# Performance work log

Measured on AMD Instinct MI355X. Metric: run time of the kernel, lower is better.

The kernel has to match this reference:

```python
import jax, jax.numpy as jnp
import numpy as np

B, N, D_IN, D_H, D_OUT, H = 16384, 32, 128, 128, 128, 4

def setup_inputs() -> dict:
    key = jax.random.key(0)
    ks = jax.random.split(key, 7)
    s_in = 1.0 / np.sqrt(D_IN)
    s_h = 1.0 / np.sqrt(D_H)
    return {
        "x": jax.random.normal(ks[0], (B, 1, D_IN), dtype=jnp.float32),
        "neighbors": jax.random.normal(ks[1], (B, N, D_IN), dtype=jnp.float32),
        "Wq": jax.random.uniform(ks[2], (H, D_H, D_IN), jnp.float32, -s_in, s_in),
        "Wk": jax.random.uniform(ks[3], (H, D_H, D_IN), jnp.float32, -s_in, s_in),
        "Wv": jax.random.uniform(ks[4], (H, D_H, D_IN), jnp.float32, -s_in, s_in),
        "Wo": jax.random.uniform(ks[5], (D_OUT, D_H), jnp.float32, -s_h, s_h),
        "bo": jax.random.uniform(ks[6], (D_OUT,), jnp.float32, -s_h, s_h),
    }

def reference(x, neighbors, Wq, Wk, Wv, Wo, bo):
    # Per-head projections (torch Linear: y = x @ W.T), batched over heads
    q = jnp.einsum("bqi,hdi->bhqd", x, Wq)          # [B,H,1,Dh]
    k = jnp.einsum("bni,hdi->bhnd", neighbors, Wk)  # [B,H,N,Dh]
    v = jnp.einsum("bni,hdi->bhnd", neighbors, Wv)  # [B,H,N,Dh]
    logits = jnp.einsum("bhqd,bhnd->bhqn", q, k)    # [B,H,1,N]
    attn = jax.nn.softmax(logits, axis=-1)
    # Sum over heads (original accumulates res += per head), then average
    res = jnp.einsum("bhqn,bhnd->bqd", attn, v) / q.shape[1]  # [B,1,Dh]
    out = jnp.einsum("bqd,od->bqo", res, Wo) + bo
    out = jax.nn.leaky_relu(out, negative_slope=0.01)
    return out[:, 0, :]  # squeeze(1) -> [B, D_OUT]
```

## Files before the change

kernel.cpp:

```cpp
#include <hip/hip_runtime.h>
#include <hip/hip_bf16.h>
#include <cstddef>

#define NBATCH 16384
#define NNB 32
#define DD 128
#define NH 4
#define NHD 512
#define NT 512
#define BPB 8

typedef __attribute__((ext_vector_type(8))) short short8v;
typedef __attribute__((ext_vector_type(4))) float f32x4;

__device__ __forceinline__ unsigned f2bf1(float f) {
  unsigned u = __float_as_uint(f);
  return (u + 0x7FFFu + ((u >> 16) & 1u)) >> 16;
}
__device__ __forceinline__ unsigned pack2bf(float lo, float hi) {
  return f2bf1(lo) | (f2bf1(hi) << 16);
}
__device__ __forceinline__ float bflo(unsigned u) { return __uint_as_float(u << 16); }
__device__ __forceinline__ float bfhi(unsigned u) { return __uint_as_float(u & 0xFFFF0000u); }

__global__ __launch_bounds__(256) void precompute_kernel(
    const float* __restrict__ Wq, const float* __restrict__ Wk,
    const float* __restrict__ Wv, const float* __restrict__ Wo,
    unsigned short* __restrict__ AAfh, unsigned short* __restrict__ AAfl,
    unsigned short* __restrict__ CCf) {
  int e = blockIdx.x * 256 + threadIdx.x;
  if (blockIdx.y == 0) {
    int i = e >> 9;
    int hd = e & 511;
    int h = hd >> 7, d = hd & 127;
    const float* wq = Wq + h * 16384;
    const float* wk = Wk + h * 16384;
    float acc = 0.f;
    #pragma unroll 8
    for (int r = 0; r < 128; ++r) acc += wq[r * 128 + i] * wk[r * 128 + d];
    int t2 = hd >> 4;
    int ks = i >> 5, kg = (i >> 3) & 3, eo = i & 7;
    int lane = (hd & 15) + 16 * kg;
    size_t idx = ((size_t)(t2 * 4 + ks) * 64 + lane) * 8 + eo;
    unsigned hv = f2bf1(acc);
    AAfh[idx] = (unsigned short)hv;
    AAfl[idx] = (unsigned short)f2bf1(acc - __uint_as_float(hv << 16));
  } else {
    int k = e >> 7;
    int o = e & 127;
    int h = k >> 7, i = k & 127;
    const float* wv = Wv + h * 16384;
    float acc = 0.f;
    #pragma unroll 8
    for (int d = 0; d < 128; ++d) acc += Wo[o * 128 + d] * wv[d * 128 + i];
    int t = o >> 4, s = k >> 5, g = (k >> 3) & 3, eo = k & 7;
    int lane = (o & 15) + 16 * g;
    size_t idx = ((size_t)(t * 16 + s) * 64 + lane) * 8 + eo;
    CCf[idx] = (unsigned short)f2bf1(0.25f * acc);
  }
}

__global__ __launch_bounds__(512) void gemm1_kernel(
    const float* __restrict__ x, const unsigned short* __restrict__ AAfh,
    const unsigned short* __restrict__ AAfl, unsigned* __restrict__ Gf32) {
  __shared__ __align__(16) float x_lds[32][132];
  const int t = threadIdx.x;
  const size_t B0 = (size_t)blockIdx.x * 32;
  {
    const float4* src = (const float4*)(x + B0 * DD);
    #pragma unroll
    for (int j = 0; j < 2; ++j) {
      int flat = j * 512 + t;
      float4 f = src[flat];
      int b = flat >> 5, c4 = flat & 31;
      *(float4*)&x_lds[b][c4 * 4] = f;
    }
  }
  __syncthreads();
  const int w = t >> 6, l = t & 63;
  const int hm = l & 15, kg = l >> 4;
  const int mt = w & 1;
  const int q = w >> 1;

  short8v xh[4], xl[4];
  #pragma unroll
  for (int ks = 0; ks < 4; ++ks) {
    float4 a = *(const float4*)&x_lds[mt * 16 + hm][ks * 32 + kg * 8];
    float4 b = *(const float4*)&x_lds[mt * 16 + hm][ks * 32 + kg * 8 + 4];
    unsigned h0 = f2bf1(a.x), h1 = f2bf1(a.y), h2 = f2bf1(a.z), h3 = f2bf1(a.w);
    unsigned h4 = f2bf1(b.x), h5 = f2bf1(b.y), h6 = f2bf1(b.z), h7 = f2bf1(b.w);
    union { unsigned u[4]; short8v v; } H, L;
    H.u[0] = h0 | (h1 << 16); H.u[1] = h2 | (h3 << 16);
    H.u[2] = h4 | (h5 << 16); H.u[3] = h6 | (h7 << 16);
    L.u[0] = pack2bf(a.x - __uint_as_float(h0 << 16), a.y - __uint_as_float(h1 << 16));
    L.u[1] = pack2bf(a.z - __uint_as_float(h2 << 16), a.w - __uint_as_float(h3 << 16));
    L.u[2] = pack2bf(b.x - __uint_as_float(h4 << 16), b.y - __uint_as_float(h5 << 16));
    L.u[3] = pack2bf(b.z - __uint_as_float(h6 << 16), b.w - __uint_as_float(h7 << 16));
    xh[ks] = H.v; xl[ks] = L.v;
  }

  #pragma unroll
  for (int tt = 0; tt < 8; ++tt) {
    const int t2 = q * 8 + tt;
    const uint4* Bh = (const uint4*)AAfh + (size_t)t2 * 256 + l;
    const uint4* Bl = (const uint4*)AAfl + (size_t)t2 * 256 + l;
    f32x4 acc = {0.f, 0.f, 0.f, 0.f};
    #pragma unroll
    for (int ks = 0; ks < 4; ++ks) {
      union { uint4 u; short8v v; } BH, BL;
      BH.u = Bh[ks * 64];
      BL.u = Bl[ks * 64];
      acc = __builtin_amdgcn_mfma_f32_16x16x32_bf16(xh[ks], BH.v, acc, 0, 0, 0);
      acc = __builtin_amdgcn_mfma_f32_16x16x32_bf16(xl[ks], BH.v, acc, 0, 0, 0);
      acc = __builtin_amdgcn_mfma_f32_16x16x32_bf16(xh[ks], BL.v, acc, 0, 0, 0);
    }
    unsigned* Gp = Gf32 + ((size_t)(blockIdx.x * 2 + mt) * 32 + t2) * 256 + l;
    #pragma unroll
    for (int r = 0; r < 4; ++r) {
      float v = acc[r];
      unsigned hv = f2bf1(v);
      unsigned lv = f2bf1(v - __uint_as_float(hv << 16));
      Gp[r * 64] = hv | (lv << 16);
    }
  }
}

__global__ __launch_bounds__(NT) void attn_kernel(
    const float* __restrict__ nb, const unsigned* __restrict__ Gf32,
    const unsigned short* __restrict__ CCf, const float* __restrict__ bo,
    float* __restrict__ out) {

  __shared__ __align__(16) unsigned short nb16[BPB][NNB][136];
  __shared__ __align__(16) unsigned ws16[BPB][260];
  __shared__ __align__(16) unsigned short at16[BPB][NNB][4];

  const int t = threadIdx.x;
  const size_t B0 = (size_t)blockIdx.x * BPB;
  const int wv = t >> 6, l = t & 63;
  const int hm = l & 15, kg = l >> 4;

  uint4 gu[4][2];
  {
    const size_t bb = B0 + wv;
    const unsigned* Gp = Gf32 + (bb >> 4) * 8192 + (size_t)(bb & 3) * 64 +
                         ((bb >> 2) & 3) * 16 + (kg & 1) * 8;
    const int t2b = (hm & 3) * 8 + (kg >> 1);
    #pragma unroll
    for (int ks = 0; ks < 4; ++ks) {
      const uint4* p = (const uint4*)(Gp + (size_t)(t2b + ks * 2) * 256);
      gu[ks][0] = p[0];
      gu[ks][1] = p[1];
    }
  }

  {
    const float4* src = (const float4*)(nb + (B0 + wv) * (NNB * DD));
    float4 va[8];
    #pragma unroll
    for (int j = 0; j < 8; ++j) va[j] = src[j * 64 + l];
    #pragma unroll
    for (int j = 0; j < 8; ++j) {
      int flat = j * 64 + l;
      int n = flat >> 5, c4 = flat & 31;
      unsigned* dst = (unsigned*)&nb16[wv][n][c4 * 4];
      dst[0] = pack2bf(va[j].x, va[j].y);
      dst[1] = pack2bf(va[j].z, va[j].w);
    }
    #pragma unroll
    for (int j = 0; j < 8; ++j) va[j] = src[(8 + j) * 64 + l];
    #pragma unroll
    for (int j = 0; j < 8; ++j) {
      int flat = (8 + j) * 64 + l;
      int n = flat >> 5, c4 = flat & 31;
      unsigned* dst = (unsigned*)&nb16[wv][n][c4 * 4];
      dst[0] = pack2bf(va[j].x, va[j].y);
      dst[1] = pack2bf(va[j].z, va[j].w);
    }
  }

  const char* nbb = (const char*)&nb16[wv][0][0];
  f32x4 acc0 = {0.f, 0.f, 0.f, 0.f}, acc1 = {0.f, 0.f, 0.f, 0.f};
  #pragma unroll
  for (int ks = 0; ks < 4; ++ks) {
    unsigned ua0 = gu[ks][0].x, ua1 = gu[ks][0].y, ua2 = gu[ks][0].z, ua3 = gu[ks][0].w;
    unsigned ua4 = gu[ks][1].x, ua5 = gu[ks][1].y, ua6 = gu[ks][1].z, ua7 = gu[ks][1].w;
    union { uint4 u; short8v v; } A0, A1, BH, BL;
    BH.u.x = (ua0 & 0xFFFFu) | (ua1 << 16);
    BH.u.y = (ua2 & 0xFFFFu) | (ua3 << 16);
    BH.u.z = (ua4 & 0xFFFFu) | (ua5 << 16);
    BH.u.w = (ua6 & 0xFFFFu) | (ua7 << 16);
    BL.u.x = (ua0 >> 16) | (ua1 & 0xFFFF0000u);
    BL.u.y = (ua2 >> 16) | (ua3 & 0xFFFF0000u);
    BL.u.z = (ua4 >> 16) | (ua5 & 0xFFFF0000u);
    BL.u.w = (ua6 >> 16) | (ua7 & 0xFFFF0000u);
    A0.u = *(const uint4*)(nbb + hm * 272 + ks * 64 + kg * 16);
    A1.u = *(const uint4*)(nbb + (16 + hm) * 272 + ks * 64 + kg * 16);
    acc0 = __builtin_amdgcn_mfma_f32_16x16x32_bf16(A0.v, BH.v, acc0, 0, 0, 0);
    acc0 = __builtin_amdgcn_mfma_f32_16x16x32_bf16(A0.v, BL.v, acc0, 0, 0, 0);
    acc1 = __builtin_amdgcn_mfma_f32_16x16x32_bf16(A1.v, BH.v, acc1, 0, 0, 0);
    acc1 = __builtin_amdgcn_mfma_f32_16x16x32_bf16(A1.v, BL.v, acc1, 0, 0, 0);
  }
  {
    float m = fmaxf(fmaxf(fmaxf(acc0[0], acc0[1]), fmaxf(acc0[2], acc0[3])),
                    fmaxf(fmaxf(acc1[0], acc1[1]), fmaxf(acc1[2], acc1[3])));
    m = fmaxf(m, __shfl_xor(m, 16));
    m = fmaxf(m, __shfl_xor(m, 32));
    float e0[4], e1[4], s = 0.f;
    #pragma unroll
    for (int r = 0; r < 4; ++r) {
      e0[r] = __expf(acc0[r] - m); s += e0[r];
      e1[r] = __expf(acc1[r] - m); s += e1[r];
    }
    s += __shfl_xor(s, 16);
    s += __shfl_xor(s, 32);
    float inv = 1.0f / s;
    if (hm < 4) {
      #pragma unroll
      for (int r = 0; r < 4; ++r) {
        at16[wv][kg * 4 + r][hm]      = (unsigned short)f2bf1(e0[r] * inv);
        at16[wv][16 + kg * 4 + r][hm] = (unsigned short)f2bf1(e1[r] * inv);
      }
    }
  }
  {
    float w00 = 0.f, w01 = 0.f, w10 = 0.f, w11 = 0.f;
    float w20 = 0.f, w21 = 0.f, w30 = 0.f, w31 = 0.f;
    #pragma unroll 8
    for (int n = 0; n < NNB; ++n) {
      unsigned u = *(const unsigned*)(nbb + n * 272 + (l << 2));
      float f0 = bflo(u), f1 = bfhi(u);
      uint2 au = *(const uint2*)&at16[wv][n][0];
      float a0 = bflo(au.x), a1 = bfhi(au.x);
      float a2 = bflo(au.y), a3 = bfhi(au.y);
      w00 += a0 * f0; w01 += a0 * f1;
      w10 += a1 * f0; w11 += a1 * f1;
      w20 += a2 * f0; w21 += a2 * f1;
      w30 += a3 * f0; w31 += a3 * f1;
    }
    ws16[wv][0 * 64 + l] = pack2bf(w00, w01);
    ws16[wv][1 * 64 + l] = pack2bf(w10, w11);
    ws16[wv][2 * 64 + l] = pack2bf(w20, w21);
    ws16[wv][3 * 64 + l] = pack2bf(w30, w31);
  }
  __syncthreads();

  {
    const int m = hm, mb = m & 7;
    f32x4 acc = {0.f, 0.f, 0.f, 0.f};
    const uint4* Bp = (const uint4*)CCf + (size_t)wv * 1024 + l;
    #pragma unroll
    for (int s = 0; s < 16; ++s) {
      union { uint4 u; short8v v; } A, B;
      A.u = *(const uint4*)&ws16[mb][s * 16 + kg * 4];
      B.u = Bp[(size_t)s * 64];
      acc = __builtin_amdgcn_mfma_f32_16x16x32_bf16(A.v, B.v, acc, 0, 0, 0);
    }
    const int o0 = wv * 16 + m;
    float bias0 = bo[o0];
    #pragma unroll
    for (int r = 0; r < 4; ++r) {
      int bat = kg * 4 + r;
      if (bat < 8) {
        float v0 = acc[r] + bias0;
        v0 = v0 > 0.f ? v0 : 0.01f * v0;
        out[(B0 + bat) * DD + o0] = v0;
      }
    }
  }
}

extern "C" void kernel_launch(void* const* d_in, const int* in_sizes, int n_in,
                              void* d_out, int out_size, void* d_ws, size_t ws_size,
                              hipStream_t stream) {
  const float* x  = (const float*)d_in[0];
  const float* nb = (const float*)d_in[1];
  const float* Wq = (const float*)d_in[2];
  const float* Wk = (const float*)d_in[3];
  const float* Wv = (const float*)d_in[4];
  const float* Wo = (const float*)d_in[5];
  const float* bo = (const float*)d_in[6];
  float* out = (float*)d_out;

  unsigned short* W = (unsigned short*)d_ws;
  unsigned short* AAfh = W;
  unsigned short* AAfl = W + 65536;
  unsigned short* CCf  = W + 131072;
  unsigned* Gf32 = (unsigned*)(W + 196608);

  precompute_kernel<<<dim3(256, 2), 256, 0, stream>>>(Wq, Wk, Wv, Wo, AAfh, AAfl, CCf);
  gemm1_kernel<<<dim3(NBATCH / 32), 512, 0, stream>>>(x, AAfh, AAfl, Gf32);
  attn_kernel<<<dim3(NBATCH / BPB), NT, 0, stream>>>(nb, Gf32, CCf, bo, out);
}
```

Measured before the change: 93.47 us.

## Load neighbors directly into MFMA fragments and use MFMA for attention-weighted sum

Drops the shared-memory bf16 staging of the neighbor tile. The logits MFMA now reads its A fragments straight from global fp32 and converts them with the hardware packed bf16 convert instruction. The scalar attention-times-neighbors loop becomes eight MFMAs fed by strided global loads, with the attention probabilities stored transposed in LDS. The weighted sums are kept in fp32 in LDS and converted at use time. This removes LDS traffic and the packing ALU work, but it reads each neighbor tile from global/L2 twice, and the second read uses strided scalar loads.

```diff
diff --git a/kernel.cpp b/kernel.cpp
--- a/kernel.cpp
+++ b/kernel.cpp
@@ -20,8 +20,11 @@
 __device__ __forceinline__ unsigned pack2bf(float lo, float hi) {
   return f2bf1(lo) | (f2bf1(hi) << 16);
 }
-__device__ __forceinline__ float bflo(unsigned u) { return __uint_as_float(u << 16); }
-__device__ __forceinline__ float bfhi(unsigned u) { return __uint_as_float(u & 0xFFFF0000u); }
+__device__ __forceinline__ unsigned cvt2(float lo, float hi) {
+  unsigned r;
+  asm("v_cvt_pk_bf16_f32 %0, %1, %2" : "=v"(r) : "v"(lo), "v"(hi));
+  return r;
+}
 
 __global__ __launch_bounds__(256) void precompute_kernel(
     const float* __restrict__ Wq, const float* __restrict__ Wk,
@@ -130,16 +133,17 @@
     const unsigned short* __restrict__ CCf, const float* __restrict__ bo,
     float* __restrict__ out) {
 
-  __shared__ __align__(16) unsigned short nb16[BPB][NNB][136];
-  __shared__ __align__(16) unsigned ws16[BPB][260];
-  __shared__ __align__(16) unsigned short at16[BPB][NNB][4];
+  __shared__ __align__(16) float ws32[BPB * 516];
+  __shared__ __align__(16) unsigned short at16T[BPB * 128];
 
   const int t = threadIdx.x;
   const size_t B0 = (size_t)blockIdx.x * BPB;
   const int wv = t >> 6, l = t & 63;
   const int hm = l & 15, kg = l >> 4;
 
-  uint4 gu[4][2];
+  const float* nbB = nb + (B0 + wv) * (NNB * DD);
+
+  f32x4 acc0 = {0.f, 0.f, 0.f, 0.f}, acc1 = {0.f, 0.f, 0.f, 0.f};
   {
     const size_t bb = B0 + wv;
     const unsigned* Gp = Gf32 + (bb >> 4) * 8192 + (size_t)(bb & 3) * 64 +
@@ -147,58 +151,31 @@
     const int t2b = (hm & 3) * 8 + (kg >> 1);
     #pragma unroll
     for (int ks = 0; ks < 4; ++ks) {
+      const float* a0p = nbB + hm * DD + ks * 32 + kg * 8;
+      float4 a0a = *(const float4*)a0p;
+      float4 a0b = *(const float4*)(a0p + 4);
+      float4 a1a = *(const float4*)(a0p + 16 * DD);
+      float4 a1b = *(const float4*)(a0p + 16 * DD + 4);
       const uint4* p = (const uint4*)(Gp + (size_t)(t2b + ks * 2) * 256);
-      gu[ks][0] = p[0];
-      gu[ks][1] = p[1];
-    }
-  }
-
-  {
-    const float4* src = (const float4*)(nb + (B0 + wv) * (NNB * DD));
-    float4 va[8];
-    #pragma unroll
-    for (int j = 0; j < 8; ++j) va[j] = src[j * 64 + l];
-    #pragma unroll
-    for (int j = 0; j < 8; ++j) {
-      int flat = j * 64 + l;
-      int n = flat >> 5, c4 = flat & 31;
-      unsigned* dst = (unsigned*)&nb16[wv][n][c4 * 4];
-      dst[0] = pack2bf(va[j].x, va[j].y);
-      dst[1] = pack2bf(va[j].z, va[j].w);
-    }
-    #pragma unroll
-    for (int j = 0; j < 8; ++j) va[j] = src[(8 + j) * 64 + l];
-    #pragma unroll
-    for (int j = 0; j < 8; ++j) {
-      int flat = (8 + j) * 64 + l;
-      int n = flat >> 5, c4 = flat & 31;
-      unsigned* dst = (unsigned*)&nb16[wv][n][c4 * 4];
-      dst[0] = pack2bf(va[j].x, va[j].y);
-      dst[1] = pack2bf(va[j].z, va[j].w);
-    }
-  }
-
-  const char* nbb = (const char*)&nb16[wv][0][0];
-  f32x4 acc0 = {0.f, 0.f, 0.f, 0.f}, acc1 = {0.f, 0.f, 0.f, 0.f};
-  #pragma unroll
-  for (int ks = 0; ks < 4; ++ks) {
-    unsigned ua0 = gu[ks][0].x, ua1 = gu[ks][0].y, ua2 = gu[ks][0].z, ua3 = gu[ks][0].w;
-    unsigned ua4 = gu[ks][1].x, ua5 = gu[ks][1].y, ua6 = gu[ks][1].z, ua7 = gu[ks][1].w;
-    union { uint4 u; short8v v; } A0, A1, BH, BL;
-    BH.u.x = (ua0 & 0xFFFFu) | (ua1 << 16);
-    BH.u.y = (ua2 & 0xFFFFu) | (ua3 << 16);
-    BH.u.z = (ua4 & 0xFFFFu) | (ua5 << 16);
-    BH.u.w = (ua6 & 0xFFFFu) | (ua7 << 16);
-    BL.u.x = (ua0 >> 16) | (ua1 & 0xFFFF0000u);
-    BL.u.y = (ua2 >> 16) | (ua3 & 0xFFFF0000u);
-    BL.u.z = (ua4 >> 16) | (ua5 & 0xFFFF0000u);
-    BL.u.w = (ua6 >> 16) | (ua7 & 0xFFFF0000u);
-    A0.u = *(const uint4*)(nbb + hm * 272 + ks * 64 + kg * 16);
-    A1.u = *(const uint4*)(nbb + (16 + hm) * 272 + ks * 64 + kg * 16);
-    acc0 = __builtin_amdgcn_mfma_f32_16x16x32_bf16(A0.v, BH.v, acc0, 0, 0, 0);
-    acc0 = __builtin_amdgcn_mfma_f32_16x16x32_bf16(A0.v, BL.v, acc0, 0, 0, 0);
-    acc1 = __builtin_amdgcn_mfma_f32_16x16x32_bf16(A1.v, BH.v, acc1, 0, 0, 0);
-    acc1 = __builtin_amdgcn_mfma_f32_16x16x32_bf16(A1.v, BL.v, acc1, 0, 0, 0);
+      uint4 g0 = p[0], g1 = p[1];
+      union { uint4 u; short8v v; } A0, A1, BH, BL;
+      A0.u.x = cvt2(a0a.x, a0a.y); A0.u.y = cvt2(a0a.z, a0a.w);
+      A0.u.z = cvt2(a0b.x, a0b.y); A0.u.w = cvt2(a0b.z, a0b.w);
+      A1.u.x = cvt2(a1a.x, a1a.y); A1.u.y = cvt2(a1a.z, a1a.w);
+      A1.u.z = cvt2(a1b.x, a1b.y); A1.u.w = cvt2(a1b.z, a1b.w);
+      BH.u.x = (g0.x & 0xFFFFu) | (g0.y << 16);
+      BH.u.y = (g0.z & 0xFFFFu) | (g0.w << 16);
+      BH.u.z = (g1.x & 0xFFFFu) | (g1.y << 16);
+      BH.u.w = (g1.z & 0xFFFFu) | (g1.w << 16);
+      BL.u.x = (g0.x >> 16) | (g0.y & 0xFFFF0000u);
+      BL.u.y = (g0.z >> 16) | (g0.w & 0xFFFF0000u);
+      BL.u.z = (g1.x >> 16) | (g1.y & 0xFFFF0000u);
+      BL.u.w = (g1.z >> 16) | (g1.w & 0xFFFF0000u);
+      acc0 = __builtin_amdgcn_mfma_f32_16x16x32_bf16(A0.v, BH.v, acc0, 0, 0, 0);
+      acc0 = __builtin_amdgcn_mfma_f32_16x16x32_bf16(A0.v, BL.v, acc0, 0, 0, 0);
+      acc1 = __builtin_amdgcn_mfma_f32_16x16x32_bf16(A1.v, BH.v, acc1, 0, 0, 0);
+      acc1 = __builtin_amdgcn_mfma_f32_16x16x32_bf16(A1.v, BL.v, acc1, 0, 0, 0);
+    }
   }
   {
     float m = fmaxf(fmaxf(fmaxf(acc0[0], acc0[1]), fmaxf(acc0[2], acc0[3])),
@@ -215,47 +192,61 @@
     s += __shfl_xor(s, 32);
     float inv = 1.0f / s;
     if (hm < 4) {
+      unsigned* atp = (unsigned*)at16T + wv * 64 + hm * 16 + kg * 2;
+      atp[0] = cvt2(e0[0] * inv, e0[1] * inv);
+      atp[1] = cvt2(e0[2] * inv, e0[3] * inv);
+      atp[8] = cvt2(e1[0] * inv, e1[1] * inv);
+      atp[9] = cvt2(e1[2] * inv, e1[3] * inv);
+    }
+  }
+  f32x4 c[8];
+  {
+    union { uint4 u; short8v v; } Afr;
+    Afr.u = *(const uint4*)&at16T[wv * 128 + (hm & 3) * 32 + kg * 8];
+    const float* bp = nbB + kg * 8 * DD + hm;
+    #pragma unroll
+    for (int t8 = 0; t8 < 8; ++t8) {
+      float f0 = bp[t8 * 16 + 0 * DD];
+      float f1 = bp[t8 * 16 + 1 * DD];
+      float f2 = bp[t8 * 16 + 2 * DD];
+      float f3 = bp[t8 * 16 + 3 * DD];
+      float f4 = bp[t8 * 16 + 4 * DD];
+      float f5 = bp[t8 * 16 + 5 * DD];
+      float f6 = bp[t8 * 16 + 6 * DD];
+      float f7 = bp[t8 * 16 + 7 * DD];
+      union { uint4 u; short8v v; } Bfr;
+      Bfr.u.x = cvt2(f0, f1); Bfr.u.y = cvt2(f2, f3);
+      Bfr.u.z = cvt2(f4, f5); Bfr.u.w = cvt2(f6, f7);
+      f32x4 z = {0.f, 0.f, 0.f, 0.f};
+      c[t8] = __builtin_amdgcn_mfma_f32_16x16x32_bf16(Afr.v, Bfr.v, z, 0, 0, 0);
+    }
+  }
+  if (kg == 0) {
+    #pragma unroll
+    for (int t8 = 0; t8 < 8; ++t8) {
       #pragma unroll
-      for (int r = 0; r < 4; ++r) {
-        at16[wv][kg * 4 + r][hm]      = (unsigned short)f2bf1(e0[r] * inv);
-        at16[wv][16 + kg * 4 + r][hm] = (unsigned short)f2bf1(e1[r] * inv);
-      }
-    }
-  }
-  {
-    float w00 = 0.f, w01 = 0.f, w10 = 0.f, w11 = 0.f;
-    float w20 = 0.f, w21 = 0.f, w30 = 0.f, w31 = 0.f;
-    #pragma unroll 8
-    for (int n = 0; n < NNB; ++n) {
-      unsigned u = *(const unsigned*)(nbb + n * 272 + (l << 2));
-      float f0 = bflo(u), f1 = bfhi(u);
-      uint2 au = *(const uint2*)&at16[wv][n][0];
-      float a0 = bflo(au.x), a1 = bfhi(au.x);
-      float a2 = bflo(au.y), a3 = bfhi(au.y);
-      w00 += a0 * f0; w01 += a0 * f1;
-      w10 += a1 * f0; w11 += a1 * f1;
-      w20 += a2 * f0; w21 += a2 * f1;
-      w30 += a3 * f0; w31 += a3 * f1;
-    }
-    ws16[wv][0 * 64 + l] = pack2bf(w00, w01);
-    ws16[wv][1 * 64 + l] = pack2bf(w10, w11);
-    ws16[wv][2 * 64 + l] = pack2bf(w20, w21);
-    ws16[wv][3 * 64 + l] = pack2bf(w30, w31);
+      for (int r = 0; r < 4; ++r)
+        ws32[wv * 516 + r * 128 + t8 * 16 + hm] = c[t8][r];
+    }
   }
   __syncthreads();
 
   {
-    const int m = hm, mb = m & 7;
+    const int mb = hm & 7;
     f32x4 acc = {0.f, 0.f, 0.f, 0.f};
     const uint4* Bp = (const uint4*)CCf + (size_t)wv * 1024 + l;
     #pragma unroll
     for (int s = 0; s < 16; ++s) {
+      const float* wp = &ws32[mb * 516 + s * 32 + kg * 8];
+      float4 wa = *(const float4*)wp;
+      float4 wb = *(const float4*)(wp + 4);
       union { uint4 u; short8v v; } A, B;
-      A.u = *(const uint4*)&ws16[mb][s * 16 + kg * 4];
+      A.u.x = cvt2(wa.x, wa.y); A.u.y = cvt2(wa.z, wa.w);
+      A.u.z = cvt2(wb.x, wb.y); A.u.w = cvt2(wb.z, wb.w);
       B.u = Bp[(size_t)s * 64];
       acc = __builtin_amdgcn_mfma_f32_16x16x32_bf16(A.v, B.v, acc, 0, 0, 0);
     }
-    const int o0 = wv * 16 + m;
+    const int o0 = wv * 16 + hm;
     float bias0 = bo[o0];
     #pragma unroll
     for (int r = 0; r < 4; ++r) {
```

New measurement: 116.6 us. 24.7% more time.

## Make attention kernel persistent over batch groups with double-buffered neighbor prefetch

Applied to the files above, without the earlier changes.

Each block of the attention kernel now loops over eight groups of eight batches instead of handling one group, and the grid shrinks by the same factor. Neighbor tiles for the next group are loaded from global memory into registers while the current group computes, then written as bf16 into a second LDS buffer. The aim is to hide HBM latency for the neighbor stream behind the MFMA and softmax work. In exchange, LDS use doubles to about 140 KB per block, limiting occupancy to one block per CU, register pressure rises, and the grid has only 256 blocks with an extra barrier per iteration.

```diff
diff --git a/kernel.cpp b/kernel.cpp
--- a/kernel.cpp
+++ b/kernel.cpp
@@ -9,6 +9,7 @@
 #define NHD 512
 #define NT 512
 #define BPB 8
+#define NITER 8
 
 typedef __attribute__((ext_vector_type(8))) short short8v;
 typedef __attribute__((ext_vector_type(4))) float f32x4;
@@ -130,39 +131,24 @@
     const unsigned short* __restrict__ CCf, const float* __restrict__ bo,
     float* __restrict__ out) {
 
-  __shared__ __align__(16) unsigned short nb16[BPB][NNB][136];
+  __shared__ __align__(16) unsigned short nb16[2][BPB][NNB][136];
   __shared__ __align__(16) unsigned ws16[BPB][260];
   __shared__ __align__(16) unsigned short at16[BPB][NNB][4];
 
   const int t = threadIdx.x;
-  const size_t B0 = (size_t)blockIdx.x * BPB;
   const int wv = t >> 6, l = t & 63;
   const int hm = l & 15, kg = l >> 4;
-
-  uint4 gu[4][2];
+  const size_t Bbase = (size_t)blockIdx.x * (NITER * BPB);
+
   {
-    const size_t bb = B0 + wv;
-    const unsigned* Gp = Gf32 + (bb >> 4) * 8192 + (size_t)(bb & 3) * 64 +
-                         ((bb >> 2) & 3) * 16 + (kg & 1) * 8;
-    const int t2b = (hm & 3) * 8 + (kg >> 1);
-    #pragma unroll
-    for (int ks = 0; ks < 4; ++ks) {
-      const uint4* p = (const uint4*)(Gp + (size_t)(t2b + ks * 2) * 256);
-      gu[ks][0] = p[0];
-      gu[ks][1] = p[1];
-    }
-  }
-
-  {
-    const float4* src = (const float4*)(nb + (B0 + wv) * (NNB * DD));
+    const float4* src = (const float4*)(nb + (Bbase + wv) * (NNB * DD));
     float4 va[8];
     #pragma unroll
     for (int j = 0; j < 8; ++j) va[j] = src[j * 64 + l];
     #pragma unroll
     for (int j = 0; j < 8; ++j) {
-      int flat = j * 64 + l;
-      int n = flat >> 5, c4 = flat & 31;
-      unsigned* dst = (unsigned*)&nb16[wv][n][c4 * 4];
+      int flat = j * 64 + l, n = flat >> 5, c4 = flat & 31;
+      unsigned* dst = (unsigned*)&nb16[0][wv][n][c4 * 4];
       dst[0] = pack2bf(va[j].x, va[j].y);
       dst[1] = pack2bf(va[j].z, va[j].w);
     }
@@ -170,102 +156,157 @@
     for (int j = 0; j < 8; ++j) va[j] = src[(8 + j) * 64 + l];
     #pragma unroll
     for (int j = 0; j < 8; ++j) {
-      int flat = (8 + j) * 64 + l;
-      int n = flat >> 5, c4 = flat & 31;
-      unsigned* dst = (unsigned*)&nb16[wv][n][c4 * 4];
+      int flat = (8 + j) * 64 + l, n = flat >> 5, c4 = flat & 31;
+      unsigned* dst = (unsigned*)&nb16[0][wv][n][c4 * 4];
       dst[0] = pack2bf(va[j].x, va[j].y);
       dst[1] = pack2bf(va[j].z, va[j].w);
     }
   }
 
-  const char* nbb = (const char*)&nb16[wv][0][0];
-  f32x4 acc0 = {0.f, 0.f, 0.f, 0.f}, acc1 = {0.f, 0.f, 0.f, 0.f};
-  #pragma unroll
-  for (int ks = 0; ks < 4; ++ks) {
-    unsigned ua0 = gu[ks][0].x, ua1 = gu[ks][0].y, ua2 = gu[ks][0].z, ua3 = gu[ks][0].w;
-    unsigned ua4 = gu[ks][1].x, ua5 = gu[ks][1].y, ua6 = gu[ks][1].z, ua7 = gu[ks][1].w;
-    union { uint4 u; short8v v; } A0, A1, BH, BL;
-    BH.u.x = (ua0 & 0xFFFFu) | (ua1 << 16);
-    BH.u.y = (ua2 & 0xFFFFu) | (ua3 << 16);
-    BH.u.z = (ua4 & 0xFFFFu) | (ua5 << 16);
-    BH.u.w = (ua6 & 0xFFFFu) | (ua7 << 16);
-    BL.u.x = (ua0 >> 16) | (ua1 & 0xFFFF0000u);
-    BL.u.y = (ua2 >> 16) | (ua3 & 0xFFFF0000u);
-    BL.u.z = (ua4 >> 16) | (ua5 & 0xFFFF0000u);
-    BL.u.w = (ua6 >> 16) | (ua7 & 0xFFFF0000u);
-    A0.u = *(const uint4*)(nbb + hm * 272 + ks * 64 + kg * 16);
-    A1.u = *(const uint4*)(nbb + (16 + hm) * 272 + ks * 64 + kg * 16);
-    acc0 = __builtin_amdgcn_mfma_f32_16x16x32_bf16(A0.v, BH.v, acc0, 0, 0, 0);
-    acc0 = __builtin_amdgcn_mfma_f32_16x16x32_bf16(A0.v, BL.v, acc0, 0, 0, 0);
-    acc1 = __builtin_amdgcn_mfma_f32_16x16x32_bf16(A1.v, BH.v, acc1, 0, 0, 0);
-    acc1 = __builtin_amdgcn_mfma_f32_16x16x32_bf16(A1.v, BL.v, acc1, 0, 0, 0);
-  }
-  {
-    float m = fmaxf(fmaxf(fmaxf(acc0[0], acc0[1]), fmaxf(acc0[2], acc0[3])),
-                    fmaxf(fmaxf(acc1[0], acc1[1]), fmaxf(acc1[2], acc1[3])));
-    m = fmaxf(m, __shfl_xor(m, 16));
-    m = fmaxf(m, __shfl_xor(m, 32));
-    float e0[4], e1[4], s = 0.f;
-    #pragma unroll
-    for (int r = 0; r < 4; ++r) {
-      e0[r] = __expf(acc0[r] - m); s += e0[r];
-      e1[r] = __expf(acc1[r] - m); s += e1[r];
-    }
-    s += __shfl_xor(s, 16);
-    s += __shfl_xor(s, 32);
-    float inv = 1.0f / s;
-    if (hm < 4) {
+  #pragma unroll 1
+  for (int it = 0; it < NITER; ++it) {
+    const int cur = it & 1;
+    const size_t B0 = Bbase + (size_t)it * BPB;
+    const char* nbb = (const char*)&nb16[cur][wv][0][0];
+    const bool pf = (it + 1 < NITER);
+    const float4* srcn = (const float4*)(nb + (B0 + BPB + wv) * (NNB * DD));
+
+    uint4 gu[4][2];
+    {
+      const size_t bb = B0 + wv;
+      const unsigned* Gp = Gf32 + (bb >> 4) * 8192 + (size_t)(bb & 3) * 64 +
+                           ((bb >> 2) & 3) * 16 + (kg & 1) * 8;
+      const int t2b = (hm & 3) * 8 + (kg >> 1);
+      #pragma unroll
+      for (int ks = 0; ks < 4; ++ks) {
+        const uint4* p = (const uint4*)(Gp + (size_t)(t2b + ks * 2) * 256);
+        gu[ks][0] = p[0];
+        gu[ks][1] = p[1];
+      }
+    }
+
+    f32x4 acc0 = {0.f, 0.f, 0.f, 0.f}, acc1 = {0.f, 0.f, 0.f, 0.f};
+    #pragma unroll
+    for (int ks = 0; ks < 4; ++ks) {
+      unsigned ua0 = gu[ks][0].x, ua1 = gu[ks][0].y, ua2 = gu[ks][0].z, ua3 = gu[ks][0].w;
+      unsigned ua4 = gu[ks][1].x, ua5 = gu[ks][1].y, ua6 = gu[ks][1].z, ua7 = gu[ks][1].w;
+      union { uint4 u; short8v v; } A0, A1, BH, BL;
+      BH.u.x = (ua0 & 0xFFFFu) | (ua1 << 16);
+      BH.u.y = (ua2 & 0xFFFFu) | (ua3 << 16);
+      BH.u.z = (ua4 & 0xFFFFu) | (ua5 << 16);
+      BH.u.w = (ua6 & 0xFFFFu) | (ua7 << 16);
+      BL.u.x = (ua0 >> 16) | (ua1 & 0xFFFF0000u);
+      BL.u.y = (ua2 >> 16) | (ua3 & 0xFFFF0000u);
+      BL.u.z = (ua4 >> 16) | (ua5 & 0xFFFF0000u);
+      BL.u.w = (ua6 >> 16) | (ua7 & 0xFFFF0000u);
+      A0.u = *(const uint4*)(nbb + hm * 272 + ks * 64 + kg * 16);
+      A1.u = *(const uint4*)(nbb + (16 + hm) * 272 + ks * 64 + kg * 16);
+      acc0 = __builtin_amdgcn_mfma_f32_16x16x32_bf16(A0.v, BH.v, acc0, 0, 0, 0);
+      acc0 = __builtin_amdgcn_mfma_f32_16x16x32_bf16(A0.v, BL.v, acc0, 0, 0, 0);
+      acc1 = __builtin_amdgcn_mfma_f32_16x16x32_bf16(A1.v, BH.v, acc1, 0, 0, 0);
+      acc1 = __builtin_amdgcn_mfma_f32_16x16x32_bf16(A1.v, BL.v, acc1, 0, 0, 0);
+    }
+    {
+      float m = fmaxf(fmaxf(fmaxf(acc0[0], acc0[1]), fmaxf(acc0[2], acc0[3])),
+                      fmaxf(fmaxf(acc1[0], acc1[1]), fmaxf(acc1[2], acc1[3])));
+      m = fmaxf(m, __shfl_xor(m, 16));
+      m = fmaxf(m, __shfl_xor(m, 32));
+      float e0[4], e1[4], s = 0.f;
       #pragma unroll
       for (int r = 0; r < 4; ++r) {
-        at16[wv][kg * 4 + r][hm]      = (unsigned short)f2bf1(e0[r] * inv);
-        at16[wv][16 + kg * 4 + r][hm] = (unsigned short)f2bf1(e1[r] * inv);
-      }
-    }
-  }
-  {
-    float w00 = 0.f, w01 = 0.f, w10 = 0.f, w11 = 0.f;
-    float w20 = 0.f, w21 = 0.f, w30 = 0.f, w31 = 0.f;
-    #pragma unroll 8
-    for (int n = 0; n < NNB; ++n) {
-      unsigned u = *(const unsigned*)(nbb + n * 272 + (l << 2));
-      float f0 = bflo(u), f1 = bfhi(u);
-      uint2 au = *(const uint2*)&at16[wv][n][0];
-      float a0 = bflo(au.x), a1 = bfhi(au.x);
-      float a2 = bflo(au.y), a3 = bfhi(au.y);
-      w00 += a0 * f0; w01 += a0 * f1;
-      w10 += a1 * f0; w11 += a1 * f1;
-      w20 += a2 * f0; w21 += a2 * f1;
-      w30 += a3 * f0; w31 += a3 * f1;
-    }
-    ws16[wv][0 * 64 + l] = pack2bf(w00, w01);
-    ws16[wv][1 * 64 + l] = pack2bf(w10, w11);
-    ws16[wv][2 * 64 + l] = pack2bf(w20, w21);
-    ws16[wv][3 * 64 + l] = pack2bf(w30, w31);
-  }
-  __syncthreads();
-
-  {
-    const int m = hm, mb = m & 7;
-    f32x4 acc = {0.f, 0.f, 0.f, 0.f};
-    const uint4* Bp = (const uint4*)CCf + (size_t)wv * 1024 + l;
-    #pragma unroll
-    for (int s = 0; s < 16; ++s) {
-      union { uint4 u; short8v v; } A, B;
-      A.u = *(const uint4*)&ws16[mb][s * 16 + kg * 4];
-      B.u = Bp[(size_t)s * 64];
-      acc = __builtin_amdgcn_mfma_f32_16x16x32_bf16(A.v, B.v, acc, 0, 0, 0);
-    }
-    const int o0 = wv * 16 + m;
-    float bias0 = bo[o0];
-    #pragma unroll
-    for (int r = 0; r < 4; ++r) {
-      int bat = kg * 4 + r;
-      if (bat < 8) {
-        float v0 = acc[r] + bias0;
-        v0 = v0 > 0.f ? v0 : 0.01f * v0;
-        out[(B0 + bat) * DD + o0] = v0;
-      }
-    }
+        e0[r] = __expf(acc0[r] - m); s += e0[r];
+        e1[r] = __expf(acc1[r] - m); s += e1[r];
+      }
+      s += __shfl_xor(s, 16);
+      s += __shfl_xor(s, 32);
+      float inv = 1.0f / s;
+      if (hm < 4) {
+        #pragma unroll
+        for (int r = 0; r < 4; ++r) {
+          at16[wv][kg * 4 + r][hm]      = (unsigned short)f2bf1(e0[r] * inv);
+          at16[wv][16 + kg * 4 + r][hm] = (unsigned short)f2bf1(e1[r] * inv);
+        }
+      }
+    }
+
+    float4 va[8];
+    if (pf) {
+      #pragma unroll
+      for (int j = 0; j < 8; ++j) va[j] = srcn[j * 64 + l];
+    }
+
+    {
+      float w00 = 0.f, w01 = 0.f, w10 = 0.f, w11 = 0.f;
+      float w20 = 0.f, w21 = 0.f, w30 = 0.f, w31 = 0.f;
+      #pragma unroll 8
+      for (int n = 0; n < NNB; ++n) {
+        unsigned u = *(const unsigned*)(nbb + n * 272 + (l << 2));
+        float f0 = bflo(u), f1 = bfhi(u);
+        uint2 au = *(const uint2*)&at16[wv][n][0];
+        float a0 = bflo(au.x), a1 = bfhi(au.x);
+        float a2 = bflo(au.y), a3 = bfhi(au.y);
+        w00 += a0 * f0; w01 += a0 * f1;
+        w10 += a1 * f0; w11 += a1 * f1;
+        w20 += a2 * f0; w21 += a2 * f1;
+        w30 += a3 * f0; w31 += a3 * f1;
+      }
+      ws16[wv][0 * 64 + l] = pack2bf(w00, w01);
+      ws16[wv][1 * 64 + l] = pack2bf(w10, w11);
+      ws16[wv][2 * 64 + l] = pack2bf(w20, w21);
+      ws16[wv][3 * 64 + l] = pack2bf(w30, w31);
+    }
+
+    if (pf) {
+      #pragma unroll
+      for (int j = 0; j < 8; ++j) {
+        int flat = j * 64 + l, n = flat >> 5, c4 = flat & 31;
+        unsigned* dst = (unsigned*)&nb16[cur ^ 1][wv][n][c4 * 4];
+        dst[0] = pack2bf(va[j].x, va[j].y);
+        dst[1] = pack2bf(va[j].z, va[j].w);
+      }
+    }
+    float4 vb[8];
+    if (pf) {
+      #pragma unroll
+      for (int j = 0; j < 8; ++j) vb[j] = srcn[(8 + j) * 64 + l];
+    }
+
+    __syncthreads();
+
+    {
+      const int m = hm, mb = m & 7;
+      f32x4 acc = {0.f, 0.f, 0.f, 0.f};
+      const uint4* Bp = (const uint4*)CCf + (size_t)wv * 1024 + l;
+      #pragma unroll
+      for (int s = 0; s < 16; ++s) {
+        union { uint4 u; short8v v; } A, B;
+        A.u = *(const uint4*)&ws16[mb][s * 16 + kg * 4];
+        B.u = Bp[(size_t)s * 64];
+        acc = __builtin_amdgcn_mfma_f32_16x16x32_bf16(A.v, B.v, acc, 0, 0, 0);
+      }
+      const int o0 = wv * 16 + m;
+      float bias0 = bo[o0];
+      #pragma unroll
+      for (int r = 0; r < 4; ++r) {
+        int bat = kg * 4 + r;
+        if (bat < 8) {
+          float v0 = acc[r] + bias0;
+          v0 = v0 > 0.f ? v0 : 0.01f * v0;
+          out[(B0 + bat) * DD + o0] = v0;
+        }
+      }
+    }
+
+    if (pf) {
+      #pragma unroll
+      for (int j = 0; j < 8; ++j) {
+        int flat = (8 + j) * 64 + l, n = flat >> 5, c4 = flat & 31;
+        unsigned* dst = (unsigned*)&nb16[cur ^ 1][wv][n][c4 * 4];
+        dst[0] = pack2bf(vb[j].x, vb[j].y);
+        dst[1] = pack2bf(vb[j].z, vb[j].w);
+      }
+    }
+    __syncthreads();
   }
 }
 
@@ -289,5 +330,5 @@
 
   precompute_kernel<<<dim3(256, 2), 256, 0, stream>>>(Wq, Wk, Wv, Wo, AAfh, AAfl, CCf);
   gemm1_kernel<<<dim3(NBATCH / 32), 512, 0, stream>>>(x, AAfh, AAfl, Gf32);
-  attn_kernel<<<dim3(NBATCH / BPB), NT, 0, stream>>>(nb, Gf32, CCf, bo, out);
-}
+  attn_kernel<<<dim3(NBATCH / (BPB * NITER)), NT, 0, stream>>>(nb, Gf32, CCf, bo, out);
+}
```

Measured after the change: 103.7 us. 1.11x slower.
